# Kernel optimization log

Measured on AMD Instinct MI355X. Metric: run time of the kernel, lower is better.

## Reference

```python
import jax, jax.numpy as jnp
import numpy as np

L, H, D, F = 4, 8, 64, 256  # layers, heads, head_dim, FAVOR feature dims (n_dims=256 in source)
DM = H * D                   # d_model = 512
EPS = 1e-6                   # fast_transformers LinearAttention eps


def _ln(x, g, b):
    m = jnp.mean(x, -1, keepdims=True)
    v = jnp.mean((x - m) ** 2, -1, keepdims=True)
    return (x - m) * jax.lax.rsqrt(v + 1e-5) * g + b


def _favor(x, omega):
    # FAVOR+ softmax-kernel feature map. x: [B,S,H,D], omega: [D, F//2]
    x = x * (D ** -0.25)  # x * sqrt(softmax_temp), softmax_temp = 1/sqrt(D)
    u = jnp.einsum('bshd,df->bshf', x, omega)
    h = jnp.sum(x * x, -1, keepdims=True) * 0.5
    return jnp.concatenate([jnp.exp(u - h), jnp.exp(-u - h)], -1) * (F ** -0.5)


def _forward(x, pos, enc_w1, enc_b1, enc_w2, enc_b2, enc_g, enc_b,
             wq, bq, wk, bk, wv, bv, wo, bo, ln1_g, ln1_b,
             w1, b1, w2, b2, ln2_g, ln2_b, omega, cls_w, cls_b, num_graphs):
    B = num_graphs
    N = x.shape[0]
    S = N // B
    # encoder MLP + LayerNorm
    h = jnp.concatenate([x, pos], axis=1)
    h = jax.nn.relu(h @ enc_w1 + enc_b1)
    h = _ln(h @ enc_w2 + enc_b2, enc_g, enc_b)
    h = h.reshape(B, S, DM)
    # fast_transformers post-norm encoder layers with linear (FAVOR) attention
    for l in range(L):
        q = (h @ wq[l] + bq[l]).reshape(B, S, H, D)
        k = (h @ wk[l] + bk[l]).reshape(B, S, H, D)
        v = (h @ wv[l] + bv[l]).reshape(B, S, H, D)
        Q = _favor(q, omega[l])  # [B,S,H,F]
        K = _favor(k, omega[l])
        kv = jnp.einsum('bshf,bshd->bhfd', K, v)                      # associative accumulation
        z = 1.0 / (jnp.einsum('bshf,bhf->bsh', Q, K.sum(axis=1)) + EPS)
        a = jnp.einsum('bshf,bhfd,bsh->bshd', Q, kv, z).reshape(B, S, DM)
        h = _ln(h + a @ wo[l] + bo[l], ln1_g[l], ln1_b[l])            # x = norm1(x + attn)
        y = jax.nn.relu(h @ w1[l] + b1[l]) @ w2[l] + b2[l]            # FFN (relu)
        h = _ln(h + y, ln2_g[l], ln2_b[l])                            # norm2(x + y)
    pooled = h.mean(axis=1)
    return pooled @ cls_w + cls_b


def setup_inputs() -> dict:
    key = jax.random.key(0)
    ks = jax.random.split(key, 16)
    B, S = 16, 1024
    N = B * S

    def w(k, shape):
        return jax.random.normal(k, shape, jnp.float32) * 0.02

    return dict(
        x=jax.random.normal(ks[0], (N, 3), jnp.float32),
        pos=jax.random.normal(ks[1], (N, 3), jnp.float32),
        enc_w1=w(ks[2], (6, DM // 2)), enc_b1=jnp.zeros((DM // 2,), jnp.float32),
        enc_w2=w(ks[3], (DM // 2, DM)), enc_b2=jnp.zeros((DM,), jnp.float32),
        enc_g=jnp.ones((DM,), jnp.float32), enc_b=jnp.zeros((DM,), jnp.float32),
        wq=w(ks[4], (L, DM, DM)), bq=jnp.zeros((L, DM), jnp.float32),
        wk=w(ks[5], (L, DM, DM)), bk=jnp.zeros((L, DM), jnp.float32),
        wv=w(ks[6], (L, DM, DM)), bv=jnp.zeros((L, DM), jnp.float32),
        wo=w(ks[7], (L, DM, DM)), bo=jnp.zeros((L, DM), jnp.float32),
        ln1_g=jnp.ones((L, DM), jnp.float32), ln1_b=jnp.zeros((L, DM), jnp.float32),
        w1=w(ks[8], (L, DM, 2 * DM)), b1=jnp.zeros((L, 2 * DM), jnp.float32),
        w2=w(ks[9], (L, 2 * DM, DM)), b2=jnp.zeros((L, DM), jnp.float32),
        ln2_g=jnp.ones((L, DM), jnp.float32), ln2_b=jnp.zeros((L, DM), jnp.float32),
        omega=jax.random.normal(ks[10], (L, D, F // 2), jnp.float32),
        cls_w=w(ks[11], (DM, 16)), cls_b=jnp.zeros((16,), jnp.float32),
        num_graphs=B,
    )


def reference(x, pos, enc_w1, enc_b1, enc_w2, enc_b2, enc_g, enc_b,
              wq, bq, wk, bk, wv, bv, wo, bo, ln1_g, ln1_b,
              w1, b1, w2, b2, ln2_g, ln2_b, omega, cls_w, cls_b, num_graphs):
    return _forward(x, pos, enc_w1, enc_b1, enc_w2, enc_b2, enc_g, enc_b,
                    wq, bq, wk, bk, wv, bv, wo, bo, ln1_g, ln1_b,
                    w1, b1, w2, b2, ln2_g, ln2_b, omega, cls_w, cls_b, num_graphs)
```

## Files before the change

### kernel.cpp

```cpp
#include <hip/hip_runtime.h>
#include <hip/hip_bf16.h>
#include <math.h>

#define NTOK 16384
#define BATCH 16
#define SEQ 1024
#define DMODEL 512
#define NHEAD 8
#define HDIM 64
#define FDIM 256
#define BH_TOT 128
#define SCALE_QK 0.3535533905932738f
#define SCALE2 0.125f
#define FSCALE 0.0625f

typedef __bf16 bf16x8_t __attribute__((ext_vector_type(8)));
typedef float f32x4_t  __attribute__((ext_vector_type(4)));
typedef unsigned short u16x8 __attribute__((ext_vector_type(8)));
typedef unsigned short u16x4 __attribute__((ext_vector_type(4)));
typedef const __attribute__((address_space(1))) char* gas_t;
typedef __attribute__((address_space(3))) char* las_t;

__device__ __forceinline__ float b2f(unsigned short u) {
    union { unsigned int i; float f; } c; c.i = ((unsigned int)u) << 16; return c.f;
}
__device__ __forceinline__ unsigned short f2bu(float f) {
    __hip_bfloat16 h = __float2bfloat16(f);
    return *(unsigned short*)&h;
}
__device__ __forceinline__ bf16x8_t u2b8(u16x8 u) {
    union { u16x8 a; bf16x8_t b; } c; c.a = u; return c.b;
}

__global__ __launch_bounds__(256) void convT_batch_kernel(
    const float* __restrict__ W, unsigned short* __restrict__ Wt, int K, int N,
    size_t in_lstride, size_t out_lstride)
{
    int l = blockIdx.z;
    W  += (size_t)l * in_lstride;
    Wt += (size_t)l * out_lstride;
    __shared__ float tile[32][33];
    int k0 = blockIdx.y * 32, n0 = blockIdx.x * 32;
    int t = threadIdx.x;
    int r = t >> 3, c4 = (t & 7) * 4;
    float4 v = *(const float4*)(W + (size_t)(k0 + r) * N + n0 + c4);
    tile[r][c4 + 0] = v.x; tile[r][c4 + 1] = v.y;
    tile[r][c4 + 2] = v.z; tile[r][c4 + 3] = v.w;
    __syncthreads();
    ushort4 o;
    o.x = f2bu(tile[c4 + 0][r]); o.y = f2bu(tile[c4 + 1][r]);
    o.z = f2bu(tile[c4 + 2][r]); o.w = f2bu(tile[c4 + 3][r]);
    *(ushort4*)(Wt + (size_t)(n0 + r) * K + k0 + c4) = o;
}

__global__ __launch_bounds__(256) void omT_kernel(
    const float* __restrict__ om, unsigned short* __restrict__ omT)
{
    int i = blockIdx.x * 256 + threadIdx.x;
    int l = i >> 13, rem = i & 8191;
    int f = rem >> 6, d = rem & 63;
    omT[(size_t)l * 8192 + f * 64 + d] = f2bu(om[(size_t)l * 8192 + d * 128 + f] * SCALE_QK);
}

__global__ __launch_bounds__(256) void enc1_kernel(
    const float* __restrict__ x, const float* __restrict__ pos,
    const float* __restrict__ w1, const float* __restrict__ b1,
    unsigned short* __restrict__ mid)
{
    int t = threadIdx.x;
    int row0 = blockIdx.x * 8;
    float w[6];
#pragma unroll
    for (int j = 0; j < 6; j++) w[j] = w1[j * 256 + t];
    float bias = b1[t];
#pragma unroll
    for (int rr = 0; rr < 8; rr++) {
        int row = row0 + rr;
        float acc = bias
            + x[row * 3 + 0] * w[0] + x[row * 3 + 1] * w[1] + x[row * 3 + 2] * w[2]
            + pos[row * 3 + 0] * w[3] + pos[row * 3 + 1] * w[4] + pos[row * 3 + 2] * w[5];
        mid[(size_t)row * 256 + t] = f2bu(fmaxf(acc, 0.f));
    }
}

template<int RELU>
__global__ __launch_bounds__(256) void gemm_bf16_kernel(
    const unsigned short* __restrict__ A, const unsigned short* __restrict__ Bt,
    const float* __restrict__ bias, unsigned short* __restrict__ C,
    int M, int K, int Nc, int nx)
{
    __shared__ __align__(16) unsigned short As[128 * 32];
    __shared__ __align__(16) unsigned short Bs[128 * 32];
    const int tid = threadIdx.x;
    const int id = blockIdx.x;
    const int xcd = id & 7, slot = id >> 3;
    const int bm = ((slot / nx) * 8 + xcd) * 128;
    const int bn = (slot % nx) * 128;
    const int wave = tid >> 6, lane = tid & 63;
    const int wr = (wave >> 1) * 64, wc = (wave & 1) * 64;
    const int lm = lane & 15, lk = (lane >> 4) * 8;

    f32x4_t acc[4][4];
#pragma unroll
    for (int i = 0; i < 4; i++)
#pragma unroll
        for (int j = 0; j < 4; j++)
            acc[i][j] = (f32x4_t){0.f, 0.f, 0.f, 0.f};

    for (int k0 = 0; k0 < K; k0 += 32) {
#pragma unroll
        for (int it = 0; it < 2; ++it) {
            int t = tid + it * 256;
            const unsigned short* gp = A + (size_t)(bm + (t >> 2)) * K + k0 + (t & 3) * 8;
            __builtin_amdgcn_global_load_lds((gas_t)(const char*)gp,
                (las_t)((char*)As + t * 16), 16, 0, 0);
        }
#pragma unroll
        for (int it = 0; it < 2; ++it) {
            int t = tid + it * 256;
            const unsigned short* gp = Bt + (size_t)(bn + (t >> 2)) * K + k0 + (t & 3) * 8;
            __builtin_amdgcn_global_load_lds((gas_t)(const char*)gp,
                (las_t)((char*)Bs + t * 16), 16, 0, 0);
        }
        __syncthreads();
        bf16x8_t af[4], bfr[4];
#pragma unroll
        for (int i = 0; i < 4; i++)
            af[i] = *(const bf16x8_t*)(As + (size_t)(wr + 16 * i + lm) * 32 + lk);
#pragma unroll
        for (int j = 0; j < 4; j++)
            bfr[j] = *(const bf16x8_t*)(Bs + (size_t)(wc + 16 * j + lm) * 32 + lk);
#pragma unroll
        for (int i = 0; i < 4; i++)
#pragma unroll
            for (int j = 0; j < 4; j++)
                acc[i][j] = __builtin_amdgcn_mfma_f32_16x16x32_bf16(af[i], bfr[j], acc[i][j], 0, 0, 0);
        __syncthreads();
    }

    const int col_l = lane & 15;
    const int row_q = (lane >> 4) * 4;
#pragma unroll
    for (int i = 0; i < 4; i++) {
#pragma unroll
        for (int j = 0; j < 4; j++) {
            int gn = bn + wc + 16 * j + col_l;
            float bsv = bias[gn];
            int gm0 = bm + wr + 16 * i + row_q;
#pragma unroll
            for (int r = 0; r < 4; r++) {
                float v = acc[i][j][r] + bsv;
                if (RELU) v = fmaxf(v, 0.f);
                C[(size_t)(gm0 + r) * Nc + gn] = f2bu(v);
            }
        }
    }
}

__global__ __launch_bounds__(256) void gemm_qkv_kernel(
    const unsigned short* __restrict__ A, const unsigned short* __restrict__ Bt,
    const float* __restrict__ bq, const float* __restrict__ bk, const float* __restrict__ bv,
    unsigned short* __restrict__ Q, unsigned short* __restrict__ Kk,
    unsigned short* __restrict__ vT)
{
    __shared__ __align__(16) unsigned short As[128 * 32];
    __shared__ __align__(16) unsigned short Bs[128 * 32];
    const int tid = threadIdx.x;
    const int id = blockIdx.x;
    const int xcd = id & 7, slot = id >> 3;
    const int bm = ((slot / 12) * 8 + xcd) * 128;
    const int bn = (slot % 12) * 128;
    const int wave = tid >> 6, lane = tid & 63;
    const int wr = (wave >> 1) * 64, wc = (wave & 1) * 64;
    const int lm = lane & 15, lk = (lane >> 4) * 8;
    const int K = DMODEL;

    f32x4_t acc[4][4];
#pragma unroll
    for (int i = 0; i < 4; i++)
#pragma unroll
        for (int j = 0; j < 4; j++)
            acc[i][j] = (f32x4_t){0.f, 0.f, 0.f, 0.f};

    for (int k0 = 0; k0 < K; k0 += 32) {
#pragma unroll
        for (int it = 0; it < 2; ++it) {
            int t = tid + it * 256;
            const unsigned short* gp = A + (size_t)(bm + (t >> 2)) * K + k0 + (t & 3) * 8;
            __builtin_amdgcn_global_load_lds((gas_t)(const char*)gp,
                (las_t)((char*)As + t * 16), 16, 0, 0);
        }
#pragma unroll
        for (int it = 0; it < 2; ++it) {
            int t = tid + it * 256;
            const unsigned short* gp = Bt + (size_t)(bn + (t >> 2)) * K + k0 + (t & 3) * 8;
            __builtin_amdgcn_global_load_lds((gas_t)(const char*)gp,
                (las_t)((char*)Bs + t * 16), 16, 0, 0);
        }
        __syncthreads();
        bf16x8_t af[4], bfr[4];
#pragma unroll
        for (int i = 0; i < 4; i++)
            af[i] = *(const bf16x8_t*)(As + (size_t)(wr + 16 * i + lm) * 32 + lk);
#pragma unroll
        for (int j = 0; j < 4; j++)
            bfr[j] = *(const bf16x8_t*)(Bs + (size_t)(wc + 16 * j + lm) * 32 + lk);
#pragma unroll
        for (int i = 0; i < 4; i++)
#pragma unroll
            for (int j = 0; j < 4; j++)
                acc[i][j] = __builtin_amdgcn_mfma_f32_16x16x32_bf16(af[i], bfr[j], acc[i][j], 0, 0, 0);
        __syncthreads();
    }

    const int sect = bn >> 9;
    const float* bias = (sect == 0) ? bq : (sect == 1) ? bk : bv;
    unsigned short* rowout = (sect == 0) ? Q : Kk;
    const int cb = bn & 511;
    const int col_l = lane & 15;
    const int row_q = (lane >> 4) * 4;
#pragma unroll
    for (int i = 0; i < 4; i++) {
#pragma unroll
        for (int j = 0; j < 4; j++) {
            int cn = cb + wc + 16 * j + col_l;
            float bsv = bias[cn];
            int gm0 = bm + wr + 16 * i + row_q;
            if (sect < 2) {
#pragma unroll
                for (int r = 0; r < 4; r++)
                    rowout[(size_t)(gm0 + r) * DMODEL + cn] = f2bu(acc[i][j][r] + bsv);
            } else {
                int bb_ = gm0 >> 10, ss = gm0 & 1023;
                int hh_ = cn >> 6, dd = cn & 63;
                u16x4 o4;
#pragma unroll
                for (int r = 0; r < 4; r++) o4[r] = f2bu(acc[i][j][r] + bsv);
                *(u16x4*)(vT + (((size_t)(bb_ * NHEAD + hh_) * HDIM + dd) * SEQ + ss)) = o4;
            }
        }
    }
}

__global__ __launch_bounds__(256) void favor_k_kv_kernel(
    const unsigned short* __restrict__ Kx,
    const unsigned short* __restrict__ vT,
    const unsigned short* __restrict__ omT,
    float* __restrict__ kvpart,
    float* __restrict__ kspart)
{
    const int bid = blockIdx.x;
    const int xcd = bid & 7, slot = bid >> 3;
    const int chunk = slot & 3;
    const int bh = (slot >> 2) * 8 + xcd;
    const int b = bh >> 3, h = bh & 7;
    const int tid = threadIdx.x;
    const int wave = tid >> 6, lane = tid & 63;
    const int lm = lane & 15, q = lane >> 4, lk = q * 8;
    const int quad4 = q * 4;
    const int wr = wave * 64;
    const int m0 = wave * 16;

    __shared__ __align__(16) unsigned short phiT[256 * 72];

    f32x4_t acc_kv[4][4];
#pragma unroll
    for (int i = 0; i < 4; i++)
#pragma unroll
        for (int j = 0; j < 4; j++)
            acc_kv[i][j] = (f32x4_t){0.f, 0.f, 0.f, 0.f};
    float ks_acc = 0.f;

    const unsigned short* vbase = vT + (size_t)bh * HDIM * SEQ;

    for (int st = 0; st < 4; ++st) {
        int s0 = chunk * 256 + st * 64;
        const unsigned short* krow = Kx + (size_t)(b * SEQ + s0 + m0 + lm) * DMODEL + h * HDIM;
        u16x8 xu0 = *(const u16x8*)(krow + lk);
        u16x8 xu1 = *(const u16x8*)(krow + 32 + lk);
        float p = 0.f;
#pragma unroll
        for (int e = 0; e < 8; e++) {
            float a = b2f(xu0[e]), c = b2f(xu1[e]);
            p += a * a + c * c;
        }
        p += __shfl_xor(p, 16, 64);
        p += __shfl_xor(p, 32, 64);
        float hred = 0.5f * SCALE2 * p;
        float hr[4];
#pragma unroll
        for (int r = 0; r < 4; r++) hr[r] = __shfl(hred, quad4 + r, 64);
        f32x4_t acc[8];
#pragma unroll
        for (int j = 0; j < 8; j++) acc[j] = (f32x4_t){0.f, 0.f, 0.f, 0.f};
        bf16x8_t af0 = u2b8(xu0), af1 = u2b8(xu1);
#pragma unroll
        for (int j = 0; j < 8; j++) {
            bf16x8_t b0 = *(const bf16x8_t*)(omT + (size_t)(j * 16 + lm) * 64 + lk);
            acc[j] = __builtin_amdgcn_mfma_f32_16x16x32_bf16(af0, b0, acc[j], 0, 0, 0);
            bf16x8_t b1 = *(const bf16x8_t*)(omT + (size_t)(j * 16 + lm) * 64 + 32 + lk);
            acc[j] = __builtin_amdgcn_mfma_f32_16x16x32_bf16(af1, b1, acc[j], 0, 0, 0);
        }
        __syncthreads();
#pragma unroll
        for (int j = 0; j < 8; j++) {
            int f = j * 16 + lm;
#pragma unroll
            for (int r = 0; r < 4; r++) {
                int m = m0 + quad4 + r;
                float u = acc[j][r];
                phiT[f * 72 + m]         = f2bu(__expf(u - hr[r]) * FSCALE);
                phiT[(f + 128) * 72 + m] = f2bu(__expf(-u - hr[r]) * FSCALE);
            }
        }
        __syncthreads();
        {
            const unsigned short* row = &phiT[tid * 72];
#pragma unroll
            for (int mm = 0; mm < 64; mm += 8) {
                u16x8 v = *(const u16x8*)(row + mm);
#pragma unroll
                for (int e = 0; e < 8; e++) ks_acc += b2f(v[e]);
            }
        }
#pragma unroll
        for (int ks = 0; ks < 2; ks++) {
            bf16x8_t af[4], bfr[4];
#pragma unroll
            for (int i = 0; i < 4; i++)
                af[i] = *(const bf16x8_t*)&phiT[(wr + 16 * i + lm) * 72 + ks * 32 + lk];
#pragma unroll
            for (int j = 0; j < 4; j++)
                bfr[j] = *(const bf16x8_t*)(vbase + (size_t)(16 * j + lm) * SEQ + s0 + ks * 32 + lk);
#pragma unroll
            for (int i = 0; i < 4; i++)
#pragma unroll
                for (int j = 0; j < 4; j++)
                    acc_kv[i][j] = __builtin_amdgcn_mfma_f32_16x16x32_bf16(af[i], bfr[j], acc_kv[i][j], 0, 0, 0);
        }
    }

    float* kp = kvpart + ((size_t)chunk * BH_TOT + bh) * HDIM * FDIM;
#pragma unroll
    for (int i = 0; i < 4; i++) {
#pragma unroll
        for (int j = 0; j < 4; j++) {
            int d = 16 * j + lm;
            int f0 = wr + 16 * i + quad4;
            *(f32x4_t*)(kp + (size_t)d * FDIM + f0) = acc_kv[i][j];
        }
    }
    kspart[(size_t)chunk * (BH_TOT * FDIM) + (size_t)bh * FDIM + tid] = ks_acc;
}

__global__ __launch_bounds__(256) void reduce_kv_kernel(
    const float* __restrict__ in_kv, const float* __restrict__ in_ks,
    unsigned short* __restrict__ out_kv, float* __restrict__ out_ks)
{
    const int NKV = BH_TOT * HDIM * FDIM;
    const int NKS = BH_TOT * FDIM;
    int i = blockIdx.x * 256 + threadIdx.x;
    if (i < NKV) {
        out_kv[i] = f2bu(in_kv[i] + in_kv[i + NKV] + in_kv[i + 2 * NKV] + in_kv[i + 3 * NKV]);
    } else {
        int j = i - NKV;
        out_ks[j] = in_ks[j] + in_ks[j + NKS] + in_ks[j + 2 * NKS] + in_ks[j + 3 * NKS];
    }
}

__global__ __launch_bounds__(256) void favor_q_attn_kernel(
    const unsigned short* __restrict__ Qx,
    const unsigned short* __restrict__ omT,
    const unsigned short* __restrict__ kvT,
    const float* __restrict__ ksum,
    unsigned short* __restrict__ outX)
{
    const int bid = blockIdx.x;
    const int xcd = bid & 7, slot = bid >> 3;
    const int sc = slot & 15;
    const int bh = (slot >> 4) * 8 + xcd;
    const int b = bh >> 3, h = bh & 7;
    const int s0 = sc * 64;
    const int tid = threadIdx.x;
    const int wave = tid >> 6, lane = tid & 63;
    const int lm = lane & 15, q = lane >> 4, lk = q * 8;
    const int quad4 = q * 4;
    const int m0 = wave * 16;

    __shared__ __align__(16) unsigned short phis[4][16 * 136];

    const float* ksb = ksum + (size_t)bh * FDIM;
    float ksp[8], ksm[8];
#pragma unroll
    for (int j = 0; j < 8; j++) {
        ksp[j] = ksb[j * 16 + lm];
        ksm[j] = ksb[128 + j * 16 + lm];
    }

    const unsigned short* qrow = Qx + (size_t)(b * SEQ + s0 + m0 + lm) * DMODEL + h * HDIM;
    u16x8 xu0 = *(const u16x8*)(qrow + lk);
    u16x8 xu1 = *(const u16x8*)(qrow + 32 + lk);
    float p = 0.f;
#pragma unroll
    for (int e = 0; e < 8; e++) {
        float a = b2f(xu0[e]), c = b2f(xu1[e]);
        p += a * a + c * c;
    }
    p += __shfl_xor(p, 16, 64);
    p += __shfl_xor(p, 32, 64);
    float hred = 0.5f * SCALE2 * p;
    float hr[4];
#pragma unroll
    for (int r = 0; r < 4; r++) hr[r] = __shfl(hred, quad4 + r, 64);

    f32x4_t acc[8];
#pragma unroll
    for (int j = 0; j < 8; j++) acc[j] = (f32x4_t){0.f, 0.f, 0.f, 0.f};
    bf16x8_t af0 = u2b8(xu0), af1 = u2b8(xu1);
#pragma unroll
    for (int j = 0; j < 8; j++) {
        bf16x8_t b0 = *(const bf16x8_t*)(omT + (size_t)(j * 16 + lm) * 64 + lk);
        acc[j] = __builtin_amdgcn_mfma_f32_16x16x32_bf16(af0, b0, acc[j], 0, 0, 0);
        bf16x8_t b1 = *(const bf16x8_t*)(omT + (size_t)(j * 16 + lm) * 64 + 32 + lk);
        acc[j] = __builtin_amdgcn_mfma_f32_16x16x32_bf16(af1, b1, acc[j], 0, 0, 0);
    }

    unsigned short* ph = phis[wave];
    unsigned int pm[8][2];
    float zp[4] = {0.f, 0.f, 0.f, 0.f};
#pragma unroll
    for (int j = 0; j < 8; j++) {
        int f = j * 16 + lm;
#pragma unroll
        for (int r = 0; r < 4; r++) {
            float u = acc[j][r];
            float pp = __expf(u - hr[r]) * FSCALE;
            float pmv = __expf(-u - hr[r]) * FSCALE;
            ph[(quad4 + r) * 136 + f] = f2bu(pp);
            unsigned short pmu = f2bu(pmv);
            if (r == 0)      pm[j][0] = pmu;
            else if (r == 1) pm[j][0] |= ((unsigned int)pmu << 16);
            else if (r == 2) pm[j][1] = pmu;
            else             pm[j][1] |= ((unsigned int)pmu << 16);
            zp[r] += pp * ksp[j] + pmv * ksm[j];
        }
    }
#pragma unroll
    for (int off = 1; off < 16; off <<= 1) {
        zp[0] += __shfl_xor(zp[0], off, 64);
        zp[1] += __shfl_xor(zp[1], off, 64);
        zp[2] += __shfl_xor(zp[2], off, 64);
        zp[3] += __shfl_xor(zp[3], off, 64);
    }
    float zinv[4];
#pragma unroll
    for (int r = 0; r < 4; r++) zinv[r] = 1.f / (zp[r] + 1e-6f);

    const unsigned short* kvbase = kvT + (size_t)bh * HDIM * FDIM;
    f32x4_t acc_o[4];
#pragma unroll
    for (int j = 0; j < 4; j++) acc_o[j] = (f32x4_t){0.f, 0.f, 0.f, 0.f};
#pragma unroll
    for (int k0 = 0; k0 < 128; k0 += 32) {
        bf16x8_t af = *(const bf16x8_t*)&ph[lm * 136 + k0 + lk];
#pragma unroll
        for (int j = 0; j < 4; j++) {
            bf16x8_t bfr = *(const bf16x8_t*)(kvbase + (size_t)(16 * j + lm) * FDIM + k0 + lk);
            acc_o[j] = __builtin_amdgcn_mfma_f32_16x16x32_bf16(af, bfr, acc_o[j], 0, 0, 0);
        }
    }
#pragma unroll
    for (int j = 0; j < 8; j++) {
        int f = j * 16 + lm;
        ph[(quad4 + 0) * 136 + f] = (unsigned short)(pm[j][0] & 0xffffu);
        ph[(quad4 + 1) * 136 + f] = (unsigned short)(pm[j][0] >> 16);
        ph[(quad4 + 2) * 136 + f] = (unsigned short)(pm[j][1] & 0xffffu);
        ph[(quad4 + 3) * 136 + f] = (unsigned short)(pm[j][1] >> 16);
    }
#pragma unroll
    for (int k0 = 0; k0 < 128; k0 += 32) {
        bf16x8_t af = *(const bf16x8_t*)&ph[lm * 136 + k0 + lk];
#pragma unroll
        for (int j = 0; j < 4; j++) {
            bf16x8_t bfr = *(const bf16x8_t*)(kvbase + (size_t)(16 * j + lm) * FDIM + 128 + k0 + lk);
            acc_o[j] = __builtin_amdgcn_mfma_f32_16x16x32_bf16(af, bfr, acc_o[j], 0, 0, 0);
        }
    }
#pragma unroll
    for (int r = 0; r < 4; r++) {
        int s = s0 + m0 + quad4 + r;
#pragma unroll
        for (int j = 0; j < 4; j++) {
            int d = 16 * j + lm;
            outX[(size_t)(b * SEQ + s) * DMODEL + h * HDIM + d] = f2bu(acc_o[j][r] * zinv[r]);
        }
    }
}

template<int HAS_RES>
__global__ __launch_bounds__(512) void add_ln_kernel(
    const unsigned short* __restrict__ res16, const unsigned short* __restrict__ tin16,
    const float* __restrict__ g, const float* __restrict__ bb,
    unsigned short* __restrict__ out16)
{
    int row = blockIdx.x, t = threadIdx.x;
    size_t idx = (size_t)row * DMODEL + t;
    float val = b2f(tin16[idx]);
    if (HAS_RES) val += b2f(res16[idx]);
    float s1 = val, s2 = val * val;
#pragma unroll
    for (int off = 32; off; off >>= 1) {
        s1 += __shfl_down(s1, off, 64);
        s2 += __shfl_down(s2, off, 64);
    }
    __shared__ float w1s[8], w2s[8];
    int wid = t >> 6, lane = t & 63;
    if (lane == 0) { w1s[wid] = s1; w2s[wid] = s2; }
    __syncthreads();
    if (t == 0) {
        float a1 = 0.f, a2 = 0.f;
#pragma unroll
        for (int i = 0; i < 8; i++) { a1 += w1s[i]; a2 += w2s[i]; }
        w1s[0] = a1 * (1.f / DMODEL);
        w2s[0] = a2 * (1.f / DMODEL);
    }
    __syncthreads();
    float m = w1s[0];
    float var = w2s[0] - m * m;
    float r = rsqrtf(var + 1e-5f);
    out16[idx] = f2bu((val - m) * r * g[t] + bb[t]);
}

__global__ __launch_bounds__(256) void pool_part_kernel(
    const unsigned short* __restrict__ h16, float* __restrict__ pbuf)
{
    int blk = blockIdx.x;
    int b = blk >> 4, ch = blk & 15;
    int t = threadIdx.x;
    int d0 = t * 2;
    float a0 = 0.f, a1 = 0.f;
    const unsigned short* base = h16 + ((size_t)(b * SEQ + ch * 64) * DMODEL) + d0;
#pragma unroll 4
    for (int s = 0; s < 64; s++) {
        ushort2 v = *(const ushort2*)(base + (size_t)s * DMODEL);
        a0 += b2f(v.x); a1 += b2f(v.y);
    }
    *(float2*)(pbuf + (size_t)blk * DMODEL + d0) = make_float2(a0, a1);
}

__global__ __launch_bounds__(512) void cls_kernel(
    const float* __restrict__ pbuf, const float* __restrict__ cls_w,
    const float* __restrict__ cls_b, float* __restrict__ out)
{
    int b = blockIdx.x, t = threadIdx.x;
    float s = 0.f;
#pragma unroll
    for (int c = 0; c < 16; c++) s += pbuf[(size_t)(b * 16 + c) * DMODEL + t];
    __shared__ float pooled[DMODEL];
    pooled[t] = s * (1.f / SEQ);
    __syncthreads();
    if (t < 16) {
        float acc = cls_b[t];
        for (int c = 0; c < DMODEL; c++) acc += pooled[c] * cls_w[c * 16 + t];
        out[b * 16 + t] = acc;
    }
}

extern "C" void kernel_launch(void* const* d_in, const int* in_sizes, int n_in,
                              void* d_out, int out_size, void* d_ws, size_t ws_size,
                              hipStream_t stream)
{
    const float* x      = (const float*)d_in[0];
    const float* pos    = (const float*)d_in[1];
    const float* enc_w1 = (const float*)d_in[2];
    const float* enc_b1 = (const float*)d_in[3];
    const float* enc_w2 = (const float*)d_in[4];
    const float* enc_b2 = (const float*)d_in[5];
    const float* enc_g  = (const float*)d_in[6];
    const float* enc_bb = (const float*)d_in[7];
    const float* wq = (const float*)d_in[8];
    const float* bq = (const float*)d_in[9];
    const float* wk = (const float*)d_in[10];
    const float* bk = (const float*)d_in[11];
    const float* wv = (const float*)d_in[12];
    const float* bv = (const float*)d_in[13];
    const float* wo = (const float*)d_in[14];
    const float* bo = (const float*)d_in[15];
    const float* ln1_g = (const float*)d_in[16];
    const float* ln1_b = (const float*)d_in[17];
    const float* w1 = (const float*)d_in[18];
    const float* b1 = (const float*)d_in[19];
    const float* w2 = (const float*)d_in[20];
    const float* b2 = (const float*)d_in[21];
    const float* ln2_g = (const float*)d_in[22];
    const float* ln2_b = (const float*)d_in[23];
    const float* omega = (const float*)d_in[24];
    const float* cls_w = (const float*)d_in[25];
    const float* cls_b = (const float*)d_in[26];
    float* out = (float*)d_out;

    const int N = NTOK;
    const int BH = BH_TOT;

    char* p = (char*)d_ws;
    unsigned short* qb16 = (unsigned short*)p; p += (size_t)N * DMODEL * 2;
    unsigned short* kb16 = (unsigned short*)p; p += (size_t)N * DMODEL * 2;
    unsigned short* vT16 = (unsigned short*)p; p += (size_t)N * DMODEL * 2;
    unsigned short* h16  = (unsigned short*)p; p += (size_t)N * DMODEL * 2;
    unsigned short* mid16 = (unsigned short*)p; p += (size_t)N * 1024 * 2;
    unsigned short* attn16 = (unsigned short*)p; p += (size_t)N * DMODEL * 2;
    float* kvpart = (float*)p;                 p += (size_t)4 * BH * HDIM * FDIM * 4;
    float* kspart = (float*)p;                 p += (size_t)4 * BH * FDIM * 4;
    unsigned short* kvT16 = (unsigned short*)p; p += (size_t)BH * HDIM * FDIM * 2;
    float* ksb = (float*)p;                    p += (size_t)BH * FDIM * 4;
    float* pbuf = (float*)p;                   p += (size_t)BATCH * 16 * DMODEL * 4;
    unsigned short* enc_w2t = (unsigned short*)p; p += (size_t)256 * 512 * 2;
    unsigned short* wqkvt = (unsigned short*)p; p += (size_t)4 * 1536 * 512 * 2;
    unsigned short* wot = (unsigned short*)p;  p += (size_t)4 * 512 * 512 * 2;
    unsigned short* w1t = (unsigned short*)p;  p += (size_t)4 * 512 * 1024 * 2;
    unsigned short* w2t = (unsigned short*)p;  p += (size_t)4 * 1024 * 512 * 2;
    unsigned short* omT = (unsigned short*)p;  p += (size_t)4 * 128 * 64 * 2;

    convT_batch_kernel<<<dim3(16, 8, 1), 256, 0, stream>>>(enc_w2, enc_w2t, 256, 512, 0, 0);
    convT_batch_kernel<<<dim3(16, 16, 4), 256, 0, stream>>>(wq, wqkvt,            512, 512, 262144, 786432);
    convT_batch_kernel<<<dim3(16, 16, 4), 256, 0, stream>>>(wk, wqkvt + 262144,   512, 512, 262144, 786432);
    convT_batch_kernel<<<dim3(16, 16, 4), 256, 0, stream>>>(wv, wqkvt + 524288,   512, 512, 262144, 786432);
    convT_batch_kernel<<<dim3(16, 16, 4), 256, 0, stream>>>(wo, wot, 512, 512, 262144, 262144);
    convT_batch_kernel<<<dim3(32, 16, 4), 256, 0, stream>>>(w1, w1t, 512, 1024, 524288, 524288);
    convT_batch_kernel<<<dim3(16, 32, 4), 256, 0, stream>>>(w2, w2t, 1024, 512, 524288, 524288);
    omT_kernel<<<128, 256, 0, stream>>>(omega, omT);

    enc1_kernel<<<N / 8, 256, 0, stream>>>(x, pos, enc_w1, enc_b1, mid16);
    gemm_bf16_kernel<0><<<4 * 128, 256, 0, stream>>>(mid16, enc_w2t, enc_b2, qb16, N, 256, 512, 4);
    add_ln_kernel<0><<<N, 512, 0, stream>>>(nullptr, qb16, enc_g, enc_bb, h16);

    const int RED_BLOCKS = (BH * HDIM * FDIM + BH * FDIM) / 256;
    for (int l = 0; l < 4; l++) {
        const unsigned short* omT_l = omT + (size_t)l * 8192;
        gemm_qkv_kernel<<<12 * 128, 256, 0, stream>>>(
            h16, wqkvt + (size_t)l * 786432,
            bq + l * DMODEL, bk + l * DMODEL, bv + l * DMODEL,
            qb16, kb16, vT16);
        favor_k_kv_kernel<<<BH * 4, 256, 0, stream>>>(kb16, vT16, omT_l, kvpart, kspart);
        reduce_kv_kernel<<<RED_BLOCKS, 256, 0, stream>>>(kvpart, kspart, kvT16, ksb);
        favor_q_attn_kernel<<<BH * 16, 256, 0, stream>>>(qb16, omT_l, kvT16, ksb, attn16);
        gemm_bf16_kernel<0><<<4 * 128, 256, 0, stream>>>(attn16, wot + (size_t)l * 262144, bo + l * DMODEL, qb16, N, 512, 512, 4);
        add_ln_kernel<1><<<N, 512, 0, stream>>>(h16, qb16, ln1_g + l * DMODEL, ln1_b + l * DMODEL, h16);
        gemm_bf16_kernel<1><<<8 * 128, 256, 0, stream>>>(h16, w1t + (size_t)l * 524288, b1 + l * 1024, mid16, N, 512, 1024, 8);
        gemm_bf16_kernel<0><<<4 * 128, 256, 0, stream>>>(mid16, w2t + (size_t)l * 524288, b2 + l * DMODEL, qb16, N, 1024, 512, 4);
        add_ln_kernel<1><<<N, 512, 0, stream>>>(h16, qb16, ln2_g + l * DMODEL, ln2_b + l * DMODEL, h16);
    }

    pool_part_kernel<<<BATCH * 16, 256, 0, stream>>>(h16, pbuf);
    cls_kernel<<<BATCH, 512, 0, stream>>>(pbuf, cls_w, cls_b, out);
}
```

Baseline: 1.196 ms.

## Vectorize LayerNorm per-wave rows, store kv partials in bf16, recompute phi-minus

LayerNorm now handles one row per wave, with 8 rows per 512-thread block, and uses 16-byte loads and stores plus shuffle-only reductions. The block-level shared-memory syncs are gone. The kv partial sums are written as bf16 instead of fp32, and the reduce kernel is vectorized to halve that traffic, at some cost in accumulation precision. The attention kernel stages ksum in shared memory and recomputes the negative feature exponentials rather than packing them in registers, trading extra exp work for lower register pressure.

```diff
diff --git a/kernel.cpp b/kernel.cpp
--- a/kernel.cpp
+++ b/kernel.cpp
@@ -246,7 +246,7 @@
     const unsigned short* __restrict__ Kx,
     const unsigned short* __restrict__ vT,
     const unsigned short* __restrict__ omT,
-    float* __restrict__ kvpart,
+    unsigned short* __restrict__ kvpart,
     float* __restrict__ kspart)
 {
     const int bid = blockIdx.x;
@@ -340,31 +340,49 @@
         }
     }
 
-    float* kp = kvpart + ((size_t)chunk * BH_TOT + bh) * HDIM * FDIM;
+    unsigned short* kp = kvpart + ((size_t)chunk * BH_TOT + bh) * HDIM * FDIM;
 #pragma unroll
     for (int i = 0; i < 4; i++) {
 #pragma unroll
         for (int j = 0; j < 4; j++) {
             int d = 16 * j + lm;
             int f0 = wr + 16 * i + quad4;
-            *(f32x4_t*)(kp + (size_t)d * FDIM + f0) = acc_kv[i][j];
+            u16x4 o4;
+#pragma unroll
+            for (int r = 0; r < 4; r++) o4[r] = f2bu(acc_kv[i][j][r]);
+            *(u16x4*)(kp + (size_t)d * FDIM + f0) = o4;
         }
     }
     kspart[(size_t)chunk * (BH_TOT * FDIM) + (size_t)bh * FDIM + tid] = ks_acc;
 }
 
 __global__ __launch_bounds__(256) void reduce_kv_kernel(
-    const float* __restrict__ in_kv, const float* __restrict__ in_ks,
+    const unsigned short* __restrict__ in_kv, const float* __restrict__ in_ks,
     unsigned short* __restrict__ out_kv, float* __restrict__ out_ks)
 {
     const int NKV = BH_TOT * HDIM * FDIM;
     const int NKS = BH_TOT * FDIM;
-    int i = blockIdx.x * 256 + threadIdx.x;
-    if (i < NKV) {
-        out_kv[i] = f2bu(in_kv[i] + in_kv[i + NKV] + in_kv[i + 2 * NKV] + in_kv[i + 3 * NKV]);
+    int blk = blockIdx.x;
+    if (blk < 1024) {
+        size_t base = ((size_t)blk * 256 + threadIdx.x) * 8;
+        u16x8 v0 = *(const u16x8*)(in_kv + base);
+        u16x8 v1 = *(const u16x8*)(in_kv + base + NKV);
+        u16x8 v2 = *(const u16x8*)(in_kv + base + 2 * (size_t)NKV);
+        u16x8 v3 = *(const u16x8*)(in_kv + base + 3 * (size_t)NKV);
+        u16x8 o;
+#pragma unroll
+        for (int e = 0; e < 8; e++)
+            o[e] = f2bu(b2f(v0[e]) + b2f(v1[e]) + b2f(v2[e]) + b2f(v3[e]));
+        *(u16x8*)(out_kv + base) = o;
     } else {
-        int j = i - NKV;
-        out_ks[j] = in_ks[j] + in_ks[j + NKS] + in_ks[j + 2 * NKS] + in_ks[j + 3 * NKS];
+        size_t j = ((size_t)(blk - 1024) * 256 + threadIdx.x) * 4;
+        float4 a0 = *(const float4*)(in_ks + j);
+        float4 a1 = *(const float4*)(in_ks + j + NKS);
+        float4 a2 = *(const float4*)(in_ks + j + 2 * (size_t)NKS);
+        float4 a3 = *(const float4*)(in_ks + j + 3 * (size_t)NKS);
+        float4 o = make_float4(a0.x + a1.x + a2.x + a3.x, a0.y + a1.y + a2.y + a3.y,
+                               a0.z + a1.z + a2.z + a3.z, a0.w + a1.w + a2.w + a3.w);
+        *(float4*)(out_ks + j) = o;
     }
 }
 
@@ -388,14 +406,9 @@
     const int m0 = wave * 16;
 
     __shared__ __align__(16) unsigned short phis[4][16 * 136];
-
-    const float* ksb = ksum + (size_t)bh * FDIM;
-    float ksp[8], ksm[8];
-#pragma unroll
-    for (int j = 0; j < 8; j++) {
-        ksp[j] = ksb[j * 16 + lm];
-        ksm[j] = ksb[128 + j * 16 + lm];
-    }
+    __shared__ __align__(16) float kss[4][256];
+
+    *(float4*)&kss[wave][lane * 4] = *(const float4*)(ksum + (size_t)bh * FDIM + lane * 4);
 
     const unsigned short* qrow = Qx + (size_t)(b * SEQ + s0 + m0 + lm) * DMODEL + h * HDIM;
     u16x8 xu0 = *(const u16x8*)(qrow + lk);
@@ -426,23 +439,18 @@
     }
 
     unsigned short* ph = phis[wave];
-    unsigned int pm[8][2];
     float zp[4] = {0.f, 0.f, 0.f, 0.f};
 #pragma unroll
     for (int j = 0; j < 8; j++) {
         int f = j * 16 + lm;
+        float ksp = kss[wave][f], ksm = kss[wave][128 + f];
 #pragma unroll
         for (int r = 0; r < 4; r++) {
             float u = acc[j][r];
             float pp = __expf(u - hr[r]) * FSCALE;
-            float pmv = __expf(-u - hr[r]) * FSCALE;
+            float pm = __expf(-u - hr[r]) * FSCALE;
             ph[(quad4 + r) * 136 + f] = f2bu(pp);
-            unsigned short pmu = f2bu(pmv);
-            if (r == 0)      pm[j][0] = pmu;
-            else if (r == 1) pm[j][0] |= ((unsigned int)pmu << 16);
-            else if (r == 2) pm[j][1] = pmu;
-            else             pm[j][1] |= ((unsigned int)pmu << 16);
-            zp[r] += pp * ksp[j] + pmv * ksm[j];
+            zp[r] += pp * ksp + pm * ksm;
         }
     }
 #pragma unroll
@@ -472,10 +480,9 @@
 #pragma unroll
     for (int j = 0; j < 8; j++) {
         int f = j * 16 + lm;
-        ph[(quad4 + 0) * 136 + f] = (unsigned short)(pm[j][0] & 0xffffu);
-        ph[(quad4 + 1) * 136 + f] = (unsigned short)(pm[j][0] >> 16);
-        ph[(quad4 + 2) * 136 + f] = (unsigned short)(pm[j][1] & 0xffffu);
-        ph[(quad4 + 3) * 136 + f] = (unsigned short)(pm[j][1] >> 16);
+#pragma unroll
+        for (int r = 0; r < 4; r++)
+            ph[(quad4 + r) * 136 + f] = f2bu(__expf(-acc[j][r] - hr[r]) * FSCALE);
     }
 #pragma unroll
     for (int k0 = 0; k0 < 128; k0 += 32) {
@@ -503,32 +510,41 @@
     const float* __restrict__ g, const float* __restrict__ bb,
     unsigned short* __restrict__ out16)
 {
-    int row = blockIdx.x, t = threadIdx.x;
-    size_t idx = (size_t)row * DMODEL + t;
-    float val = b2f(tin16[idx]);
-    if (HAS_RES) val += b2f(res16[idx]);
-    float s1 = val, s2 = val * val;
-#pragma unroll
-    for (int off = 32; off; off >>= 1) {
-        s1 += __shfl_down(s1, off, 64);
-        s2 += __shfl_down(s2, off, 64);
-    }
-    __shared__ float w1s[8], w2s[8];
-    int wid = t >> 6, lane = t & 63;
-    if (lane == 0) { w1s[wid] = s1; w2s[wid] = s2; }
-    __syncthreads();
-    if (t == 0) {
-        float a1 = 0.f, a2 = 0.f;
-#pragma unroll
-        for (int i = 0; i < 8; i++) { a1 += w1s[i]; a2 += w2s[i]; }
-        w1s[0] = a1 * (1.f / DMODEL);
-        w2s[0] = a2 * (1.f / DMODEL);
-    }
-    __syncthreads();
-    float m = w1s[0];
-    float var = w2s[0] - m * m;
+    int wave = threadIdx.x >> 6, lane = threadIdx.x & 63;
+    int row = blockIdx.x * 8 + wave;
+    size_t base = (size_t)row * DMODEL + lane * 8;
+    u16x8 tv = *(const u16x8*)(tin16 + base);
+    float v[8];
+    float s1 = 0.f, s2 = 0.f;
+    if (HAS_RES) {
+        u16x8 rv = *(const u16x8*)(res16 + base);
+#pragma unroll
+        for (int e = 0; e < 8; e++) v[e] = b2f(tv[e]) + b2f(rv[e]);
+    } else {
+#pragma unroll
+        for (int e = 0; e < 8; e++) v[e] = b2f(tv[e]);
+    }
+#pragma unroll
+    for (int e = 0; e < 8; e++) { s1 += v[e]; s2 += v[e] * v[e]; }
+#pragma unroll
+    for (int off = 1; off < 64; off <<= 1) {
+        s1 += __shfl_xor(s1, off, 64);
+        s2 += __shfl_xor(s2, off, 64);
+    }
+    float m = s1 * (1.f / DMODEL);
+    float var = s2 * (1.f / DMODEL) - m * m;
     float r = rsqrtf(var + 1e-5f);
-    out16[idx] = f2bu((val - m) * r * g[t] + bb[t]);
+    float4 g0 = *(const float4*)(g + lane * 8);
+    float4 g1 = *(const float4*)(g + lane * 8 + 4);
+    float4 b0 = *(const float4*)(bb + lane * 8);
+    float4 b1 = *(const float4*)(bb + lane * 8 + 4);
+    float gg[8] = {g0.x, g0.y, g0.z, g0.w, g1.x, g1.y, g1.z, g1.w};
+    float bbv[8] = {b0.x, b0.y, b0.z, b0.w, b1.x, b1.y, b1.z, b1.w};
+    u16x8 o;
+#pragma unroll
+    for (int e = 0; e < 8; e++)
+        o[e] = f2bu((v[e] - m) * r * gg[e] + bbv[e]);
+    *(u16x8*)(out16 + base) = o;
 }
 
 __global__ __launch_bounds__(256) void pool_part_kernel(
@@ -609,7 +625,7 @@
     unsigned short* h16  = (unsigned short*)p; p += (size_t)N * DMODEL * 2;
     unsigned short* mid16 = (unsigned short*)p; p += (size_t)N * 1024 * 2;
     unsigned short* attn16 = (unsigned short*)p; p += (size_t)N * DMODEL * 2;
-    float* kvpart = (float*)p;                 p += (size_t)4 * BH * HDIM * FDIM * 4;
+    unsigned short* kvpart = (unsigned short*)p; p += (size_t)4 * BH * HDIM * FDIM * 2;
     float* kspart = (float*)p;                 p += (size_t)4 * BH * FDIM * 4;
     unsigned short* kvT16 = (unsigned short*)p; p += (size_t)BH * HDIM * FDIM * 2;
     float* ksb = (float*)p;                    p += (size_t)BH * FDIM * 4;
@@ -632,9 +648,8 @@
 
     enc1_kernel<<<N / 8, 256, 0, stream>>>(x, pos, enc_w1, enc_b1, mid16);
     gemm_bf16_kernel<0><<<4 * 128, 256, 0, stream>>>(mid16, enc_w2t, enc_b2, qb16, N, 256, 512, 4);
-    add_ln_kernel<0><<<N, 512, 0, stream>>>(nullptr, qb16, enc_g, enc_bb, h16);
-
-    const int RED_BLOCKS = (BH * HDIM * FDIM + BH * FDIM) / 256;
+    add_ln_kernel<0><<<N / 8, 512, 0, stream>>>(nullptr, qb16, enc_g, enc_bb, h16);
+
     for (int l = 0; l < 4; l++) {
         const unsigned short* omT_l = omT + (size_t)l * 8192;
         gemm_qkv_kernel<<<12 * 128, 256, 0, stream>>>(
@@ -642,13 +657,13 @@
             bq + l * DMODEL, bk + l * DMODEL, bv + l * DMODEL,
             qb16, kb16, vT16);
         favor_k_kv_kernel<<<BH * 4, 256, 0, stream>>>(kb16, vT16, omT_l, kvpart, kspart);
-        reduce_kv_kernel<<<RED_BLOCKS, 256, 0, stream>>>(kvpart, kspart, kvT16, ksb);
+        reduce_kv_kernel<<<1056, 256, 0, stream>>>(kvpart, kspart, kvT16, ksb);
         favor_q_attn_kernel<<<BH * 16, 256, 0, stream>>>(qb16, omT_l, kvT16, ksb, attn16);
         gemm_bf16_kernel<0><<<4 * 128, 256, 0, stream>>>(attn16, wot + (size_t)l * 262144, bo + l * DMODEL, qb16, N, 512, 512, 4);
-        add_ln_kernel<1><<<N, 512, 0, stream>>>(h16, qb16, ln1_g + l * DMODEL, ln1_b + l * DMODEL, h16);
+        add_ln_kernel<1><<<N / 8, 512, 0, stream>>>(h16, qb16, ln1_g + l * DMODEL, ln1_b + l * DMODEL, h16);
         gemm_bf16_kernel<1><<<8 * 128, 256, 0, stream>>>(h16, w1t + (size_t)l * 524288, b1 + l * 1024, mid16, N, 512, 1024, 8);
         gemm_bf16_kernel<0><<<4 * 128, 256, 0, stream>>>(mid16, w2t + (size_t)l * 524288, b2 + l * DMODEL, qb16, N, 1024, 512, 4);
-        add_ln_kernel<1><<<N, 512, 0, stream>>>(h16, qb16, ln2_g + l * DMODEL, ln2_b + l * DMODEL, h16);
+        add_ln_kernel<1><<<N / 8, 512, 0, stream>>>(h16, qb16, ln2_g + l * DMODEL, ln2_b + l * DMODEL, h16);
     }
 
     pool_part_kernel<<<BATCH * 16, 256, 0, stream>>>(h16, pbuf);
```

After: 1.045 ms (median of 2 runs). -12.6%, faster.
